# Performance work log

Measured on AMD Instinct MI355X. Metric: run time of the kernel, lower is better.

## Reference

```python
import jax, jax.numpy as jnp
import numpy as np

B, C, Np, D = 16, 64, 128, 128
HT = 4      # time heads
HS = 4      # space heads (GAT)
F = D       # GAT out_channels
DK = D // 2 # q/k proj dim
TOPK = 8
NEG = -1e30

def ln(x, g, b):
    m = x.mean(-1, keepdims=True)
    v = jnp.mean((x - m) ** 2, axis=-1, keepdims=True)
    return (x - m) / jnp.sqrt(v + 1e-5) * g + b

def setup_inputs() -> dict:
    key = jax.random.key(0)
    ks = jax.random.split(key, 16)
    w = lambda k, s: (jax.random.normal(k, s, jnp.float32) * 0.02)
    return dict(
        H_in=jax.random.normal(ks[0], (B, C, Np, D), jnp.float32),
        static_adj=jax.random.normal(ks[1], (C, C), jnp.float32) * 0.1,
        attn_in_w=w(ks[2], (3 * D, D)), attn_in_b=jnp.zeros((3 * D,), jnp.float32),
        attn_out_w=w(ks[3], (D, D)), attn_out_b=jnp.zeros((D,), jnp.float32),
        ln1_g=jnp.ones((D,), jnp.float32), ln1_b=jnp.zeros((D,), jnp.float32),
        ln2_g=jnp.ones((D,), jnp.float32), ln2_b=jnp.zeros((D,), jnp.float32),
        ff1_w=w(ks[4], (4 * D, D)), ff1_b=jnp.zeros((4 * D,), jnp.float32),
        ff2_w=w(ks[5], (D, 4 * D)), ff2_b=jnp.zeros((D,), jnp.float32),
        tnorm_g=jnp.ones((D,), jnp.float32), tnorm_b=jnp.zeros((D,), jnp.float32),
        q_w=w(ks[6], (DK, D)), q_b=jnp.zeros((DK,), jnp.float32),
        k_w=w(ks[7], (DK, D)), k_b=jnp.zeros((DK,), jnp.float32),
        gat_w=w(ks[8], (HS, F, D)),
        gat_att_src=w(ks[9], (HS, F)), gat_att_dst=w(ks[10], (HS, F)),
        gat_bias=jnp.zeros((D,), jnp.float32),
        snorm_g=jnp.ones((D,), jnp.float32), snorm_b=jnp.zeros((D,), jnp.float32),
    )

def _forward(H_in, static_adj, attn_in_w, attn_in_b, attn_out_w, attn_out_b,
             ln1_g, ln1_b, ln2_g, ln2_b, ff1_w, ff1_b, ff2_w, ff2_b,
             tnorm_g, tnorm_b, q_w, q_b, k_w, k_b,
             gat_w, gat_att_src, gat_att_dst, gat_bias, snorm_g, snorm_b):
    dh = D // HT
    # ---- temporal transformer encoder layer (norm_first) on [B*C, Np, D]
    x0 = H_in.reshape(B * C, Np, D)
    h = ln(x0, ln1_g, ln1_b)
    qkv = h @ attn_in_w.T + attn_in_b
    q, k, v = jnp.split(qkv, 3, axis=-1)
    q = q.reshape(-1, Np, HT, dh).transpose(0, 2, 1, 3)
    k = k.reshape(-1, Np, HT, dh).transpose(0, 2, 1, 3)
    v = v.reshape(-1, Np, HT, dh).transpose(0, 2, 1, 3)
    att = jax.nn.softmax(jnp.einsum('nhqd,nhkd->nhqk', q, k) / jnp.sqrt(jnp.float32(dh)), axis=-1)
    o = jnp.einsum('nhqk,nhkd->nhqd', att, v).transpose(0, 2, 1, 3).reshape(-1, Np, D)
    x = x0 + (o @ attn_out_w.T + attn_out_b)
    h2 = ln(x, ln2_g, ln2_b)
    x = x + jax.nn.relu(h2 @ ff1_w.T + ff1_b) @ ff2_w.T + ff2_b
    H_temp = ln(x0 + x, tnorm_g, tnorm_b).reshape(B, C, Np, D)
    # ---- dynamic adjacency from temporal summary
    Hs = H_temp.mean(axis=2)                              # [B,C,D]
    q2 = Hs @ q_w.T + q_b
    k2 = Hs @ k_w.T + k_b
    sim = jnp.einsum('bcd,bed->bce', q2, k2) * (DK ** -0.5)
    A = jnp.tanh(sim) + static_adj[None]                  # [B,C,C]
    # ---- top-k edge mask per sample (row r -> its top-k cols, no self loops)
    kk = max(1, min(TOPK, C - 1))
    idx = jax.lax.top_k(A, kk)[1]                         # [B,C,kk]
    mask = jnp.any(jax.nn.one_hot(idx, C, dtype=bool), axis=2)  # [B,C,C]
    mask = mask & (~jnp.eye(C, dtype=bool)) & (A != 0)
    # ---- dense masked GAT over all (B, Np) graphs; src=row, dst=col
    xh = jnp.einsum('bcpd,hfd->bphcf', H_temp, gat_w)     # [B,Np,HS,C,F]
    asrc = jnp.einsum('bphcf,hf->bphc', xh, gat_att_src)
    adst = jnp.einsum('bphcf,hf->bphc', xh, gat_att_dst)
    e = asrc[..., :, None] + adst[..., None, :]           # [B,Np,HS,src,dst]
    e = jnp.where(e > 0, e, 0.2 * e)                      # LeakyReLU(0.2)
    mb = mask[:, None, None, :, :]
    e = jnp.where(mb, e, NEG)
    e = e - e.max(axis=3, keepdims=True)                  # softmax over src per dst
    wgt = jnp.exp(e) * mb
    s = wgt.sum(axis=3, keepdims=True)
    a = wgt / jnp.where(s > 0, s, 1.0)
    out = jnp.einsum('bphst,bphsf->bphtf', a, xh).mean(axis=2) + gat_bias  # [B,Np,C,F]
    out = out.transpose(0, 2, 1, 3)                       # [B,C,Np,D]
    return ln(out + H_temp, snorm_g, snorm_b)

def reference(H_in, static_adj, attn_in_w, attn_in_b, attn_out_w, attn_out_b,
              ln1_g, ln1_b, ln2_g, ln2_b, ff1_w, ff1_b, ff2_w, ff2_b,
              tnorm_g, tnorm_b, q_w, q_b, k_w, k_b,
              gat_w, gat_att_src, gat_att_dst, gat_bias, snorm_g, snorm_b):
    return _forward(H_in, static_adj, attn_in_w, attn_in_b, attn_out_w, attn_out_b,
                    ln1_g, ln1_b, ln2_g, ln2_b, ff1_w, ff1_b, ff2_w, ff2_b,
                    tnorm_g, tnorm_b, q_w, q_b, k_w, k_b,
                    gat_w, gat_att_src, gat_att_dst, gat_bias, snorm_g, snorm_b)
```

## Files before the change

kernel.cpp:

```cpp
#include <hip/hip_runtime.h>
#include <cstdint>


typedef __attribute__((ext_vector_type(8)))  short bf16x8;
typedef __attribute__((ext_vector_type(16))) float f32x16;
#define MFMA32(a, b, c) __builtin_amdgcn_mfma_f32_32x32x16_bf16((a), (b), (c), 0, 0, 0)

__device__ __forceinline__ unsigned short f2bf(float f) {
    unsigned int u = __float_as_uint(f);
    u += 0x7fffu + ((u >> 16) & 1u);
    return (unsigned short)(u >> 16);
}
__device__ __forceinline__ float bf2f(unsigned short u) {
    return __uint_as_float(((unsigned int)u) << 16);
}

__device__ __forceinline__ bf16x8 lds_frag(const unsigned short* p) {
    union { bf16x8 v; ushort4 h[2]; } u;
    u.h[0] = *(const ushort4*)p;
    u.h[1] = *(const ushort4*)(p + 4);
    return u.v;
}
__device__ __forceinline__ bf16x8 gfrag(const unsigned short* p) {
    union { bf16x8 v; uint4 u; } t;
    t.u = *(const uint4*)p;
    return t.v;
}

__device__ __forceinline__ int rowmap(int r, int hl) { return (r & 3) + 8 * (r >> 2) + 4 * hl; }

__device__ __forceinline__ unsigned int pk2(float lo, float hi) {
    return (unsigned int)f2bf(lo) | ((unsigned int)f2bf(hi) << 16);
}

template<int B>
__device__ __forceinline__ bf16x8 pack_frag(const f32x16& p) {
    unsigned int a0 = pk2(p[B + 0], p[B + 1]);
    unsigned int a1 = pk2(p[B + 2], p[B + 3]);
    unsigned int b0 = pk2(p[B + 4], p[B + 5]);
    unsigned int b1 = pk2(p[B + 6], p[B + 7]);
    asm("v_permlane32_swap_b32 %0, %1" : "+v"(b0), "+v"(a0));
    asm("v_permlane32_swap_b32 %0, %1" : "+v"(b1), "+v"(a1));
    union { bf16x8 v; unsigned int w[4]; } u;
    u.w[0] = a0; u.w[1] = a1; u.w[2] = b0; u.w[3] = b1;
    return u.v;
}

__global__ void wconv_kernel(const float* __restrict__ wqkv, const float* __restrict__ wout,
                             const float* __restrict__ w1, const float* __restrict__ w2,
                             const float* __restrict__ gw,
                             unsigned short* __restrict__ dst) {
    int i = blockIdx.x * 256 + threadIdx.x;
    float v;
    if (i < 49152)       v = wqkv[i];
    else if (i < 65536)  v = wout[i - 49152];
    else if (i < 131072) v = w1[i - 65536];
    else if (i < 196608) v = w2[i - 131072];
    else                 v = gw[i - 196608];
    dst[i] = f2bf(v);
}

__global__ void wa_kernel(const float* __restrict__ gw, const float* __restrict__ asw,
                          const float* __restrict__ adw,
                          float* __restrict__ waS, float* __restrict__ waD) {
    int t = blockIdx.x * 256 + threadIdx.x;
    int h = t >> 8, d = (t >> 1) & 127, which = t & 1;
    const float* av = which ? adw : asw;
    float s = 0.f;
    for (int f = 0; f < 128; f++) s += av[h * 128 + f] * gw[(h * 128 + f) * 128 + d];
    (which ? waD : waS)[h * 128 + d] = s;
}

__global__ __launch_bounds__(256, 2)
void temporal_kernel(const float* __restrict__ Hin,
                     const unsigned short* __restrict__ wqkv_b, const float* __restrict__ bqkv,
                     const unsigned short* __restrict__ wout_b, const float* __restrict__ bout,
                     const float* __restrict__ g1, const float* __restrict__ b1,
                     const float* __restrict__ g2, const float* __restrict__ b2,
                     const unsigned short* __restrict__ w1_b, const float* __restrict__ bf1,
                     const unsigned short* __restrict__ w2_b, const float* __restrict__ bf2,
                     const float* __restrict__ tg, const float* __restrict__ tb,
                     float* __restrict__ Htemp) {
    __shared__ unsigned short RA[128][132];
    __shared__ double RBd[2208];
    unsigned short (*kb)[36]  = (unsigned short(*)[36])RBd;
    unsigned short (*vT)[132] = (unsigned short(*)[132])((char*)RBd + 9216);
    unsigned short (*rscr)[32][36] = (unsigned short(*)[32][36])RBd;

    const int n = blockIdx.x;
    const int tid = threadIdx.x;
    const int lane = tid & 63;
    const int wv = tid >> 6;
    const int hl = lane >> 5;
    const int l31 = lane & 31;
    const int myrow = wv * 32 + l31;

    {
        int row = tid >> 1, hf = tid & 1;
        const float* src = Hin + ((long)n * 128 + row) * 128 + hf * 64;
        float xv[64];
        float s = 0.f, qs = 0.f;
#pragma unroll
        for (int i = 0; i < 64; i += 4) {
            float4 t = *(const float4*)(src + i);
            xv[i] = t.x; xv[i+1] = t.y; xv[i+2] = t.z; xv[i+3] = t.w;
        }
#pragma unroll
        for (int i = 0; i < 64; i++) { s += xv[i]; qs += xv[i] * xv[i]; }
        s += __shfl_xor(s, 1); qs += __shfl_xor(qs, 1);
        float mu = s * 0.0078125f;
        float rs = rsqrtf(fmaxf(qs * 0.0078125f - mu * mu, 0.f) + 1e-5f);
#pragma unroll
        for (int i = 0; i < 64; i++) {
            int d = hf * 64 + i;
            RA[row][d] = f2bf((xv[i] - mu) * rs * g1[d] + b1[d]);
        }
    }

    unsigned int opk[4][8];

#pragma unroll
    for (int h = 0; h < 4; h++) {
        bf16x8 qf0, qf1;
        {
            f32x16 accq, acck, accv;
#pragma unroll
            for (int r = 0; r < 16; r++) accq[r] = bqkv[h * 32 + rowmap(r, hl)];
            float bk = bqkv[128 + h * 32 + l31];
            float bv = bqkv[256 + h * 32 + l31];
#pragma unroll
            for (int r = 0; r < 16; r++) { acck[r] = bk; accv[r] = bv; }
            const unsigned short* wq = wqkv_b + (      h * 32 + l31) * 128 + hl * 8;
            const unsigned short* wk = wqkv_b + (128 + h * 32 + l31) * 128 + hl * 8;
            const unsigned short* wvp= wqkv_b + (256 + h * 32 + l31) * 128 + hl * 8;
#pragma unroll
            for (int k0 = 0; k0 < 128; k0 += 16) {
                bf16x8 a  = lds_frag(&RA[myrow][k0 + hl * 8]);
                accq = MFMA32(gfrag(wq + k0), a, accq);
                acck = MFMA32(a, gfrag(wk + k0), acck);
                accv = MFMA32(a, gfrag(wvp + k0), accv);
            }
#pragma unroll
            for (int r = 0; r < 16; r++) {
                int tok = wv * 32 + rowmap(r, hl);
                kb[tok][l31] = f2bf(acck[r]);
                vT[l31][tok] = f2bf(accv[r]);
            }
            qf0 = pack_frag<0>(accq);
            qf1 = pack_frag<8>(accq);
        }
        __syncthreads();

        f32x16 sacc[4];
#pragma unroll
        for (int t = 0; t < 4; t++)
#pragma unroll
            for (int r = 0; r < 16; r++) sacc[t][r] = 0.f;
#pragma unroll
        for (int t = 0; t < 4; t++) {
            bf16x8 ka0 = lds_frag(&kb[t * 32 + l31][hl * 8]);
            sacc[t] = MFMA32(ka0, qf0, sacc[t]);
            bf16x8 ka1 = lds_frag(&kb[t * 32 + l31][16 + hl * 8]);
            sacc[t] = MFMA32(ka1, qf1, sacc[t]);
        }
        const float scale = 0.17677669529663687f;
        float m0 = -1e30f;
#pragma unroll
        for (int t = 0; t < 4; t++)
#pragma unroll
            for (int r = 0; r < 16; r++) m0 = fmaxf(m0, sacc[t][r]);
        m0 = fmaxf(m0, __shfl_xor(m0, 32));
        float ssum = 0.f;
#pragma unroll
        for (int t = 0; t < 4; t++)
#pragma unroll
            for (int r = 0; r < 16; r++) {
                float e = __expf(scale * (sacc[t][r] - m0));
                sacc[t][r] = e; ssum += e;
            }
        ssum += __shfl_xor(ssum, 32);
        float rinv = 1.f / ssum;
#pragma unroll
        for (int t = 0; t < 4; t++)
#pragma unroll
            for (int r = 0; r < 16; r++) sacc[t][r] *= rinv;

        f32x16 oacc;
#pragma unroll
        for (int r = 0; r < 16; r++) oacc[r] = 0.f;
#pragma unroll
        for (int t = 0; t < 4; t++) {
            bf16x8 pf0 = pack_frag<0>(sacc[t]);
            bf16x8 v0  = lds_frag(&vT[l31][t * 32 + hl * 8]);
            oacc = MFMA32(pf0, v0, oacc);
            bf16x8 pf1 = pack_frag<8>(sacc[t]);
            bf16x8 v1  = lds_frag(&vT[l31][t * 32 + 16 + hl * 8]);
            oacc = MFMA32(pf1, v1, oacc);
        }
#pragma unroll
        for (int j = 0; j < 8; j++) opk[h][j] = pk2(oacc[2*j], oacc[2*j+1]);
        __syncthreads();
    }

#pragma unroll
    for (int h = 0; h < 4; h++)
#pragma unroll
        for (int j = 0; j < 8; j++) {
            int tok0 = wv * 32 + rowmap(2*j,     hl);
            int tok1 = wv * 32 + rowmap(2*j + 1, hl);
            RA[tok0][h * 32 + l31] = (unsigned short)(opk[h][j] & 0xffffu);
            RA[tok1][h * 32 + l31] = (unsigned short)(opk[h][j] >> 16);
        }

    f32x16 acc[4];
#pragma unroll
    for (int t = 0; t < 4; t++) {
        float bo = bout[t * 32 + l31];
#pragma unroll
        for (int r = 0; r < 16; r++) {
            int tok = wv * 32 + rowmap(r, hl);
            acc[t][r] = Hin[((long)n * 128 + tok) * 128 + t * 32 + l31] + bo;
        }
    }
#pragma unroll
    for (int k0 = 0; k0 < 128; k0 += 16) {
        bf16x8 a = lds_frag(&RA[myrow][k0 + hl * 8]);
#pragma unroll
        for (int t = 0; t < 4; t++) {
            bf16x8 b = gfrag(wout_b + (t * 32 + l31) * 128 + k0 + hl * 8);
            acc[t] = MFMA32(a, b, acc[t]);
        }
    }

#pragma unroll
    for (int r = 0; r < 16; r++) {
        float s = acc[0][r] + acc[1][r] + acc[2][r] + acc[3][r];
#pragma unroll
        for (int d = 1; d < 32; d <<= 1) s += __shfl_xor(s, d);
        float mu = s * 0.0078125f;
        float q = 0.f;
#pragma unroll
        for (int t = 0; t < 4; t++) { float dv = acc[t][r] - mu; q += dv * dv; }
#pragma unroll
        for (int d = 1; d < 32; d <<= 1) q += __shfl_xor(q, d);
        float rs = rsqrtf(q * 0.0078125f + 1e-5f);
        int row = wv * 32 + rowmap(r, hl);
#pragma unroll
        for (int t = 0; t < 4; t++) {
            int col = t * 32 + l31;
            RA[row][col] = f2bf((acc[t][r] - mu) * rs * g2[col] + b2[col]);
        }
    }

#pragma unroll
    for (int t = 0; t < 4; t++) {
        float bv = bf2[t * 32 + l31];
#pragma unroll
        for (int r = 0; r < 16; r++) acc[t][r] += bv;
    }

    for (int j = 0; j < 4; j++) {
        f32x16 racc[4];
#pragma unroll
        for (int t = 0; t < 4; t++) {
            float bv = bf1[j * 128 + t * 32 + l31];
#pragma unroll
            for (int r = 0; r < 16; r++) racc[t][r] = bv;
        }
#pragma unroll
        for (int k0 = 0; k0 < 128; k0 += 16) {
            bf16x8 a = lds_frag(&RA[myrow][k0 + hl * 8]);
#pragma unroll
            for (int t = 0; t < 4; t++) {
                bf16x8 b = gfrag(w1_b + (j * 128 + t * 32 + l31) * 128 + k0 + hl * 8);
                racc[t] = MFMA32(a, b, racc[t]);
            }
        }
#pragma unroll
        for (int t = 0; t < 4; t++) {
#pragma unroll
            for (int r = 0; r < 16; r++)
                rscr[wv][rowmap(r, hl)][l31] = f2bf(fmaxf(racc[t][r], 0.f));
#pragma unroll
            for (int kk = 0; kk < 32; kk += 16) {
                bf16x8 a = lds_frag(&rscr[wv][l31][kk + hl * 8]);
#pragma unroll
                for (int tp = 0; tp < 4; tp++) {
                    bf16x8 b = gfrag(w2_b + (tp * 32 + l31) * 512 + j * 128 + t * 32 + kk + hl * 8);
                    acc[tp] = MFMA32(a, b, acc[tp]);
                }
            }
        }
    }

#pragma unroll
    for (int t = 0; t < 4; t++)
#pragma unroll
        for (int r = 0; r < 16; r++) {
            int tok = wv * 32 + rowmap(r, hl);
            acc[t][r] += Hin[((long)n * 128 + tok) * 128 + t * 32 + l31];
        }
    float* outf = Htemp + (long)n * 16384;
#pragma unroll
    for (int r = 0; r < 16; r++) {
        float s = acc[0][r] + acc[1][r] + acc[2][r] + acc[3][r];
#pragma unroll
        for (int d = 1; d < 32; d <<= 1) s += __shfl_xor(s, d);
        float mu = s * 0.0078125f;
        float q = 0.f;
#pragma unroll
        for (int t = 0; t < 4; t++) { float dv = acc[t][r] - mu; q += dv * dv; }
#pragma unroll
        for (int d = 1; d < 32; d <<= 1) q += __shfl_xor(q, d);
        float rs = rsqrtf(q * 0.0078125f + 1e-5f);
        int tok = wv * 32 + rowmap(r, hl);
#pragma unroll
        for (int t = 0; t < 4; t++) {
            int col = t * 32 + l31;
            outf[tok * 128 + col] = (acc[t][r] - mu) * rs * tg[col] + tb[col];
        }
    }
}

__global__ void hs_kernel(const float* __restrict__ Htemp, float* __restrict__ Hs) {
    int idx = blockIdx.x * 256 + threadIdx.x;
    int n = idx >> 7, d = idx & 127;
    float s = 0.f;
    for (int p = 0; p < 128; p++) s += Htemp[((long)n * 128 + p) * 128 + d];
    Hs[idx] = s * 0.0078125f;
}

__global__ __launch_bounds__(256)
void graph_kernel(const float* __restrict__ Hs,
                  const float* __restrict__ qw, const float* __restrict__ qb,
                  const float* __restrict__ kw, const float* __restrict__ kb,
                  const float* __restrict__ adj, unsigned long long* __restrict__ masks) {
    __shared__ float q2l[64][65];
    __shared__ float k2l[64][65];
    __shared__ float am[64][65];
    int b = blockIdx.x;
    int tid = threadIdx.x;
    {
        int r = tid & 127, jh = tid >> 7;
        int row = r & 63;
        const float* wmat = (r < 64) ? qw : kw;
        const float* bvec = (r < 64) ? qb : kb;
        const float* src = Hs + (long)(b * 64 + row) * 128;
        for (int jj = 0; jj < 32; jj++) {
            int j = jh * 32 + jj;
            const float* wrow = wmat + (long)j * 128;
            float s0 = 0.f, s1 = 0.f, s2 = 0.f, s3 = 0.f;
#pragma unroll
            for (int d = 0; d < 128; d += 4) {
                s0 += src[d] * wrow[d];     s1 += src[d+1] * wrow[d+1];
                s2 += src[d+2] * wrow[d+2]; s3 += src[d+3] * wrow[d+3];
            }
            float val = ((s0 + s1) + (s2 + s3)) + bvec[j];
            if (r < 64) q2l[row][j] = val; else k2l[row][j] = val;
        }
    }
    __syncthreads();
    {
        int c = tid & 63, eq = tid >> 6;
        for (int ee = 0; ee < 16; ee++) {
            int e = eq * 16 + ee;
            float s0 = 0.f, s1 = 0.f, s2 = 0.f, s3 = 0.f;
#pragma unroll
            for (int j = 0; j < 64; j += 4) {
                s0 += q2l[c][j]   * k2l[e][j];
                s1 += q2l[c][j+1] * k2l[e][j+1];
                s2 += q2l[c][j+2] * k2l[e][j+2];
                s3 += q2l[c][j+3] * k2l[e][j+3];
            }
            float sim = ((s0 + s1) + (s2 + s3)) * 0.125f;
            am[c][e] = tanhf(sim) + adj[c * 64 + e];
        }
    }
    __syncthreads();
    if (tid < 64) {
        int c = tid;
        unsigned long long sel = 0ull;
        for (int it = 0; it < 8; it++) {
            float best = -1e38f; int bi = 0;
            for (int e = 0; e < 64; e++) {
                float v = am[c][e];
                bool ok = (((sel >> e) & 1ull) == 0ull) && (v > best);
                best = ok ? v : best;
                bi = ok ? e : bi;
            }
            sel |= (1ull << bi);
        }
        sel &= ~(1ull << c);
        for (int e = 0; e < 64; e++)
            if (am[c][e] == 0.f) sel &= ~(1ull << e);
        masks[b * 64 + c] = sel;
    }
}

__global__ __launch_bounds__(256, 1)
void gat_kernel(float* __restrict__ Htemp,
                const unsigned short* __restrict__ gwb,
                const float* __restrict__ waS, const float* __restrict__ waD,
                const float* __restrict__ gbias,
                const unsigned long long* __restrict__ masks,
                const float* __restrict__ sg, const float* __restrict__ sb) {
    __shared__ unsigned short Htb[64][132];
    __shared__ double ovl_d[3264];
    __shared__ float asrcF[4][64], adstF[4][64];
    __shared__ float pmax[4][64], psum[4][64];
    __shared__ unsigned long long mk[64];

    unsigned short (*xhT)[68]  = (unsigned short(*)[68])ovl_d;
    unsigned short (*attT)[68] = (unsigned short(*)[68])((char*)ovl_d + 17408);
    float (*part)[8][64]       = (float(*)[8][64])ovl_d;

    const int bp = blockIdx.x;
    const int b = bp >> 7, p = bp & 127;
    const int tid = threadIdx.x;
    const int lane = tid & 63, wv = tid >> 6;
    const int hl = lane >> 5, l31 = lane & 31;
    const int rs = (wv & 1) * 32;
    const int cs = (wv >> 1) * 64;

    {
        int c = tid >> 2, qq = tid & 3;
        const float* src = Htemp + ((long)(b * 64 + c) * 128 + p) * 128 + qq * 32;
#pragma unroll
        for (int k = 0; k < 8; k++) {
            float4 t4 = *(const float4*)(src + 4 * k);
            ushort4 u; u.x = f2bf(t4.x); u.y = f2bf(t4.y); u.z = f2bf(t4.z); u.w = f2bf(t4.w);
            *(ushort4*)&Htb[c][qq * 32 + 4 * k] = u;
        }
    }
    if (tid < 64) mk[tid] = masks[b * 64 + tid];
    __syncthreads();

    {
        int s = lane, q = wv;
        float acc[8];
#pragma unroll
        for (int m = 0; m < 8; m++) acc[m] = 0.f;
        const unsigned int* hp = (const unsigned int*)&Htb[s][q * 32];
#pragma unroll
        for (int d2 = 0; d2 < 16; d2++) {
            unsigned int u = hp[d2];
            float f0 = __uint_as_float(u << 16);
            float f1 = __uint_as_float(u & 0xffff0000u);
            int d = q * 32 + 2 * d2;
#pragma unroll
            for (int h = 0; h < 4; h++) {
                acc[2*h]   += f0 * waS[h * 128 + d] + f1 * waS[h * 128 + d + 1];
                acc[2*h+1] += f0 * waD[h * 128 + d] + f1 * waD[h * 128 + d + 1];
            }
        }
#pragma unroll
        for (int m = 0; m < 8; m++) part[q][m][s] = acc[m];
    }
    __syncthreads();
    for (int o = tid; o < 512; o += 256) {
        int h = o >> 7, rem = o & 127, which = rem >> 6, s = rem & 63;
        int m = h * 2 + which;
        float v = part[0][m][s] + part[1][m][s] + part[2][m][s] + part[3][m][s];
        if (which == 0) asrcF[h][s] = v; else adstF[h][s] = v;
    }
    __syncthreads();

    f32x16 oacc0, oacc1;
#pragma unroll
    for (int r = 0; r < 16; r++) { oacc0[r] = 0.f; oacc1[r] = 0.f; }

    for (int h = 0; h < 4; h++) {
        f32x16 a0, a1;
#pragma unroll
        for (int r = 0; r < 16; r++) { a0[r] = 0.f; a1[r] = 0.f; }
        const unsigned short* gwh = gwb + h * 16384;
#pragma unroll
        for (int k0 = 0; k0 < 128; k0 += 16) {
            bf16x8 af = lds_frag(&Htb[rs + l31][k0 + hl * 8]);
            bf16x8 b0 = gfrag(gwh + (cs + l31) * 128 + k0 + hl * 8);
            bf16x8 b1 = gfrag(gwh + (cs + 32 + l31) * 128 + k0 + hl * 8);
            a0 = MFMA32(af, b0, a0);
            a1 = MFMA32(af, b1, a1);
        }
#pragma unroll
        for (int g = 0; g < 4; g++) {
            ushort4 u0, u1;
            u0.x = f2bf(a0[4*g]);   u0.y = f2bf(a0[4*g+1]);
            u0.z = f2bf(a0[4*g+2]); u0.w = f2bf(a0[4*g+3]);
            u1.x = f2bf(a1[4*g]);   u1.y = f2bf(a1[4*g+1]);
            u1.z = f2bf(a1[4*g+2]); u1.w = f2bf(a1[4*g+3]);
            int so = rs + 4 * hl + 8 * g;
            *(ushort4*)&xhT[cs + l31][so]      = u0;
            *(ushort4*)&xhT[cs + 32 + l31][so] = u1;
        }
        __syncthreads();

        {
            int t = lane;
            float adv = adstF[h][t];
            float ev[16];
            float mx = -1e30f;
#pragma unroll
            for (int i = 0; i < 16; i++) {
                int s = wv * 16 + i;
                float e = asrcF[h][s] + adv;
                e = (e > 0.f) ? e : 0.2f * e;
                ev[i] = e;
                if ((mk[s] >> t) & 1ull) mx = fmaxf(mx, e);
            }
            pmax[wv][t] = mx;
            __syncthreads();
            float M = fmaxf(fmaxf(pmax[0][t], pmax[1][t]), fmaxf(pmax[2][t], pmax[3][t]));
            float sm = 0.f;
#pragma unroll
            for (int i = 0; i < 16; i++) {
                int s = wv * 16 + i;
                float w = ((mk[s] >> t) & 1ull) ? __expf(ev[i] - M) : 0.f;
                ev[i] = w; sm += w;
            }
            psum[wv][t] = sm;
            __syncthreads();
            float S = psum[0][t] + psum[1][t] + psum[2][t] + psum[3][t];
            float rinv = (S > 0.f) ? 1.f / S : 0.f;
#pragma unroll
            for (int g = 0; g < 4; g++) {
                ushort4 u;
                u.x = f2bf(ev[4*g]   * rinv); u.y = f2bf(ev[4*g+1] * rinv);
                u.z = f2bf(ev[4*g+2] * rinv); u.w = f2bf(ev[4*g+3] * rinv);
                *(ushort4*)&attT[t][wv * 16 + 4 * g] = u;
            }
        }
        __syncthreads();

#pragma unroll
        for (int k0 = 0; k0 < 64; k0 += 16) {
            bf16x8 af = lds_frag(&attT[rs + l31][k0 + hl * 8]);
            bf16x8 b0 = lds_frag(&xhT[cs + l31][k0 + hl * 8]);
            bf16x8 b1 = lds_frag(&xhT[cs + 32 + l31][k0 + hl * 8]);
            oacc0 = MFMA32(af, b0, oacc0);
            oacc1 = MFMA32(af, b1, oacc1);
        }
        __syncthreads();
    }

    float gb0 = gbias[cs + l31], gb1 = gbias[cs + 32 + l31];
    float v0[16], v1[16];
#pragma unroll
    for (int r = 0; r < 16; r++) {
        int c = rs + rowmap(r, hl);
        v0[r] = oacc0[r] * 0.25f + gb0 + bf2f(Htb[c][cs + l31]);
        v1[r] = oacc1[r] * 0.25f + gb1 + bf2f(Htb[c][cs + 32 + l31]);
    }
#pragma unroll
    for (int r = 0; r < 16; r++) {
        float s = v0[r] + v1[r];
        float q = v0[r] * v0[r] + v1[r] * v1[r];
#pragma unroll
        for (int d = 1; d < 32; d <<= 1) { s += __shfl_xor(s, d); q += __shfl_xor(q, d); }
        if (l31 == 0) {
            int c = rs + rowmap(r, hl);
            pmax[wv >> 1][c] = s;
            psum[wv >> 1][c] = q;
        }
    }
    __syncthreads();
    float sgv0 = sg[cs + l31], sbv0 = sb[cs + l31];
    float sgv1 = sg[cs + 32 + l31], sbv1 = sb[cs + 32 + l31];
#pragma unroll
    for (int r = 0; r < 16; r++) {
        int c = rs + rowmap(r, hl);
        float sum = pmax[0][c] + pmax[1][c];
        float sq  = psum[0][c] + psum[1][c];
        float mu = sum * 0.0078125f;
        float var = sq * 0.0078125f - mu * mu;
        float rsd = rsqrtf(fmaxf(var, 0.f) + 1e-5f);
        float* orow = Htemp + ((long)(b * 64 + c) * 128 + p) * 128;
        orow[cs + l31]      = (v0[r] - mu) * rsd * sgv0 + sbv0;
        orow[cs + 32 + l31] = (v1[r] - mu) * rsd * sgv1 + sbv1;
    }
}

extern "C" void kernel_launch(void* const* d_in, const int* in_sizes, int n_in,
                              void* d_out, int out_size, void* d_ws, size_t ws_size,
                              hipStream_t stream) {
    const float* Hin        = (const float*)d_in[0];
    const float* static_adj = (const float*)d_in[1];
    const float* attn_in_w  = (const float*)d_in[2];
    const float* attn_in_b  = (const float*)d_in[3];
    const float* attn_out_w = (const float*)d_in[4];
    const float* attn_out_b = (const float*)d_in[5];
    const float* ln1_g      = (const float*)d_in[6];
    const float* ln1_b      = (const float*)d_in[7];
    const float* ln2_g      = (const float*)d_in[8];
    const float* ln2_b      = (const float*)d_in[9];
    const float* ff1_w      = (const float*)d_in[10];
    const float* ff1_b      = (const float*)d_in[11];
    const float* ff2_w      = (const float*)d_in[12];
    const float* ff2_b      = (const float*)d_in[13];
    const float* tnorm_g    = (const float*)d_in[14];
    const float* tnorm_b    = (const float*)d_in[15];
    const float* q_w        = (const float*)d_in[16];
    const float* q_b        = (const float*)d_in[17];
    const float* k_w        = (const float*)d_in[18];
    const float* k_b        = (const float*)d_in[19];
    const float* gat_w      = (const float*)d_in[20];
    const float* gat_att_src= (const float*)d_in[21];
    const float* gat_att_dst= (const float*)d_in[22];
    const float* gat_bias   = (const float*)d_in[23];
    const float* snorm_g    = (const float*)d_in[24];
    const float* snorm_b    = (const float*)d_in[25];

    float* out = (float*)d_out;
    char* ws = (char*)d_ws;
    unsigned short* wb = (unsigned short*)ws;
    const unsigned short* wqkv_b = wb;
    const unsigned short* wout_b = wb + 49152;
    const unsigned short* w1_b   = wb + 65536;
    const unsigned short* w2_b   = wb + 131072;
    const unsigned short* gw_b   = wb + 196608;
    unsigned long long* masks = (unsigned long long*)(ws + 524288);
    float* Hs  = (float*)(ws + 532480);
    float* waS = (float*)(ws + 1056768);
    float* waD = (float*)(ws + 1058816);

    hipLaunchKernelGGL(wconv_kernel, dim3(1024), dim3(256), 0, stream,
                       attn_in_w, attn_out_w, ff1_w, ff2_w, gat_w, wb);
    hipLaunchKernelGGL(wa_kernel, dim3(4), dim3(256), 0, stream,
                       gat_w, gat_att_src, gat_att_dst, waS, waD);
    hipLaunchKernelGGL(temporal_kernel, dim3(1024), dim3(256), 0, stream,
                       Hin, wqkv_b, attn_in_b, wout_b, attn_out_b,
                       ln1_g, ln1_b, ln2_g, ln2_b,
                       w1_b, ff1_b, w2_b, ff2_b, tnorm_g, tnorm_b, out);
    hipLaunchKernelGGL(hs_kernel, dim3(512), dim3(256), 0, stream, out, Hs);
    hipLaunchKernelGGL(graph_kernel, dim3(16), dim3(256), 0, stream,
                       Hs, q_w, q_b, k_w, k_b, static_adj, masks);
    hipLaunchKernelGGL(gat_kernel, dim3(2048), dim3(256), 0, stream,
                       out, gw_b, waS, waD, gat_bias,
                       masks, snorm_g, snorm_b);
}
```

Before: 576.9 us.

## Double-buffer per-head QKV with attention and fuse time-mean into temporal kernel

The per-head loop in the temporal kernel now uses two K/V LDS buffers, so the QKV projection for the next head is issued while the current head's softmax and PV run, and one barrier per head is dropped. The token mean (Hs) is computed inside the temporal epilogue through a small LDS reduction, which removes the separate hs_kernel pass that re-read all of Htemp. The GAT kernel's launch bounds are raised to two blocks per CU. In exchange, LDS use and register pressure in the temporal kernel go up, which could lower occupancy or cause spills.

```diff
diff --git a/kernel.cpp b/kernel.cpp
--- a/kernel.cpp
+++ b/kernel.cpp
@@ -71,6 +71,71 @@
     (which ? waD : waS)[h * 128 + d] = s;
 }
 
+#define QKV_STAGE(H, KBB, VTB) do {                                              \
+    f32x16 accq, acck, accv;                                                     \
+    _Pragma("unroll") for (int r = 0; r < 16; r++)                               \
+        accq[r] = bqkv[(H) * 32 + rowmap(r, hl)];                                \
+    float bk_ = bqkv[128 + (H) * 32 + l31];                                      \
+    float bv_ = bqkv[256 + (H) * 32 + l31];                                      \
+    _Pragma("unroll") for (int r = 0; r < 16; r++) { acck[r] = bk_; accv[r] = bv_; } \
+    const unsigned short* wq_ = wqkv_b + ((H) * 32 + l31) * 128 + hl * 8;        \
+    const unsigned short* wk_ = wqkv_b + (128 + (H) * 32 + l31) * 128 + hl * 8;  \
+    const unsigned short* wv_ = wqkv_b + (256 + (H) * 32 + l31) * 128 + hl * 8;  \
+    _Pragma("unroll") for (int k0 = 0; k0 < 128; k0 += 16) {                     \
+        bf16x8 a_ = lds_frag(&RA[myrow][k0 + hl * 8]);                           \
+        accq = MFMA32(gfrag(wq_ + k0), a_, accq);   \
+        acck = MFMA32(a_, gfrag(wk_ + k0), acck);                                \
+        accv = MFMA32(a_, gfrag(wv_ + k0), accv);                                \
+    }                                                                            \
+    _Pragma("unroll") for (int r = 0; r < 16; r++) {                             \
+        int tok_ = wv * 32 + rowmap(r, hl);                                      \
+        KBB[tok_][l31] = f2bf(acck[r]);                                          \
+        VTB[l31][tok_] = f2bf(accv[r]);                                          \
+    }                                                                            \
+    qf0_ = pack_frag<0>(accq);                                                   \
+    qf1_ = pack_frag<8>(accq);                                                   \
+} while (0)
+
+#define ATTN_PHASE(H, KBB, VTB, NEXTQKV) do {                                    \
+    f32x16 sacc[4];                                                              \
+    _Pragma("unroll") for (int t = 0; t < 4; t++)                                \
+    _Pragma("unroll") for (int r = 0; r < 16; r++) sacc[t][r] = 0.f;             \
+    _Pragma("unroll") for (int t = 0; t < 4; t++) {                              \
+        bf16x8 ka0 = lds_frag(&KBB[t * 32 + l31][hl * 8]);                       \
+        sacc[t] = MFMA32(ka0, qf0_, sacc[t]);                                    \
+        bf16x8 ka1 = lds_frag(&KBB[t * 32 + l31][16 + hl * 8]);                  \
+        sacc[t] = MFMA32(ka1, qf1_, sacc[t]);                                    \
+    }                                                                            \
+    NEXTQKV;                                                                     \
+    const float scale_ = 0.17677669529663687f;                   \
+    float m0 = -1e30f;                                                           \
+    _Pragma("unroll") for (int t = 0; t < 4; t++)                                \
+    _Pragma("unroll") for (int r = 0; r < 16; r++) m0 = fmaxf(m0, sacc[t][r]);   \
+    m0 = fmaxf(m0, __shfl_xor(m0, 32));                                          \
+    float ssum = 0.f;                                                            \
+    _Pragma("unroll") for (int t = 0; t < 4; t++)                                \
+    _Pragma("unroll") for (int r = 0; r < 16; r++) {                             \
+        float e_ = __expf(scale_ * (sacc[t][r] - m0));                           \
+        sacc[t][r] = e_; ssum += e_;                                             \
+    }                                                                            \
+    ssum += __shfl_xor(ssum, 32);                                                \
+    float rinv_ = 1.f / ssum;                                                    \
+    _Pragma("unroll") for (int t = 0; t < 4; t++)                                \
+    _Pragma("unroll") for (int r = 0; r < 16; r++) sacc[t][r] *= rinv_;          \
+    f32x16 oacc;                                                                 \
+    _Pragma("unroll") for (int r = 0; r < 16; r++) oacc[r] = 0.f;                \
+    _Pragma("unroll") for (int t = 0; t < 4; t++) {                              \
+        bf16x8 pf0 = pack_frag<0>(sacc[t]);                                      \
+        bf16x8 v0_ = lds_frag(&VTB[l31][t * 32 + hl * 8]);                       \
+        oacc = MFMA32(pf0, v0_, oacc);                                           \
+        bf16x8 pf1 = pack_frag<8>(sacc[t]);                                      \
+        bf16x8 v1_ = lds_frag(&VTB[l31][t * 32 + 16 + hl * 8]);                  \
+        oacc = MFMA32(pf1, v1_, oacc);                                           \
+    }                                                                            \
+    _Pragma("unroll") for (int j = 0; j < 8; j++)                                \
+        opk[H][j] = pk2(oacc[2*j], oacc[2*j+1]);                                 \
+} while (0)
+
 __global__ __launch_bounds__(256, 2)
 void temporal_kernel(const float* __restrict__ Hin,
                      const unsigned short* __restrict__ wqkv_b, const float* __restrict__ bqkv,
@@ -80,12 +145,15 @@
                      const unsigned short* __restrict__ w1_b, const float* __restrict__ bf1,
                      const unsigned short* __restrict__ w2_b, const float* __restrict__ bf2,
                      const float* __restrict__ tg, const float* __restrict__ tb,
-                     float* __restrict__ Htemp) {
+                     float* __restrict__ Htemp, float* __restrict__ Hs) {
     __shared__ unsigned short RA[128][132];
-    __shared__ double RBd[2208];
-    unsigned short (*kb)[36]  = (unsigned short(*)[36])RBd;
-    unsigned short (*vT)[132] = (unsigned short(*)[132])((char*)RBd + 9216);
+    __shared__ double RBd[4416];
+    unsigned short (*kb0)[36]  = (unsigned short(*)[36])RBd;
+    unsigned short (*vT0)[132] = (unsigned short(*)[132])((char*)RBd + 9216);
+    unsigned short (*kb1)[36]  = (unsigned short(*)[36])((char*)RBd + 17664);
+    unsigned short (*vT1)[132] = (unsigned short(*)[132])((char*)RBd + 26880);
     unsigned short (*rscr)[32][36] = (unsigned short(*)[32][36])RBd;
+    float (*hsred)[128] = (float(*)[128])((char*)RBd + 9216);
 
     const int n = blockIdx.x;
     const int tid = threadIdx.x;
@@ -118,89 +186,17 @@
     }
 
     unsigned int opk[4][8];
-
-#pragma unroll
-    for (int h = 0; h < 4; h++) {
-        bf16x8 qf0, qf1;
-        {
-            f32x16 accq, acck, accv;
-#pragma unroll
-            for (int r = 0; r < 16; r++) accq[r] = bqkv[h * 32 + rowmap(r, hl)];
-            float bk = bqkv[128 + h * 32 + l31];
-            float bv = bqkv[256 + h * 32 + l31];
-#pragma unroll
-            for (int r = 0; r < 16; r++) { acck[r] = bk; accv[r] = bv; }
-            const unsigned short* wq = wqkv_b + (      h * 32 + l31) * 128 + hl * 8;
-            const unsigned short* wk = wqkv_b + (128 + h * 32 + l31) * 128 + hl * 8;
-            const unsigned short* wvp= wqkv_b + (256 + h * 32 + l31) * 128 + hl * 8;
-#pragma unroll
-            for (int k0 = 0; k0 < 128; k0 += 16) {
-                bf16x8 a  = lds_frag(&RA[myrow][k0 + hl * 8]);
-                accq = MFMA32(gfrag(wq + k0), a, accq);
-                acck = MFMA32(a, gfrag(wk + k0), acck);
-                accv = MFMA32(a, gfrag(wvp + k0), accv);
-            }
-#pragma unroll
-            for (int r = 0; r < 16; r++) {
-                int tok = wv * 32 + rowmap(r, hl);
-                kb[tok][l31] = f2bf(acck[r]);
-                vT[l31][tok] = f2bf(accv[r]);
-            }
-            qf0 = pack_frag<0>(accq);
-            qf1 = pack_frag<8>(accq);
-        }
-        __syncthreads();
-
-        f32x16 sacc[4];
-#pragma unroll
-        for (int t = 0; t < 4; t++)
-#pragma unroll
-            for (int r = 0; r < 16; r++) sacc[t][r] = 0.f;
-#pragma unroll
-        for (int t = 0; t < 4; t++) {
-            bf16x8 ka0 = lds_frag(&kb[t * 32 + l31][hl * 8]);
-            sacc[t] = MFMA32(ka0, qf0, sacc[t]);
-            bf16x8 ka1 = lds_frag(&kb[t * 32 + l31][16 + hl * 8]);
-            sacc[t] = MFMA32(ka1, qf1, sacc[t]);
-        }
-        const float scale = 0.17677669529663687f;
-        float m0 = -1e30f;
-#pragma unroll
-        for (int t = 0; t < 4; t++)
-#pragma unroll
-            for (int r = 0; r < 16; r++) m0 = fmaxf(m0, sacc[t][r]);
-        m0 = fmaxf(m0, __shfl_xor(m0, 32));
-        float ssum = 0.f;
-#pragma unroll
-        for (int t = 0; t < 4; t++)
-#pragma unroll
-            for (int r = 0; r < 16; r++) {
-                float e = __expf(scale * (sacc[t][r] - m0));
-                sacc[t][r] = e; ssum += e;
-            }
-        ssum += __shfl_xor(ssum, 32);
-        float rinv = 1.f / ssum;
-#pragma unroll
-        for (int t = 0; t < 4; t++)
-#pragma unroll
-            for (int r = 0; r < 16; r++) sacc[t][r] *= rinv;
-
-        f32x16 oacc;
-#pragma unroll
-        for (int r = 0; r < 16; r++) oacc[r] = 0.f;
-#pragma unroll
-        for (int t = 0; t < 4; t++) {
-            bf16x8 pf0 = pack_frag<0>(sacc[t]);
-            bf16x8 v0  = lds_frag(&vT[l31][t * 32 + hl * 8]);
-            oacc = MFMA32(pf0, v0, oacc);
-            bf16x8 pf1 = pack_frag<8>(sacc[t]);
-            bf16x8 v1  = lds_frag(&vT[l31][t * 32 + 16 + hl * 8]);
-            oacc = MFMA32(pf1, v1, oacc);
-        }
-#pragma unroll
-        for (int j = 0; j < 8; j++) opk[h][j] = pk2(oacc[2*j], oacc[2*j+1]);
-        __syncthreads();
-    }
+    bf16x8 qf0_, qf1_;
+
+    QKV_STAGE(0, kb0, vT0);
+    __syncthreads();
+    ATTN_PHASE(0, kb0, vT0, QKV_STAGE(1, kb1, vT1));
+    __syncthreads();
+    ATTN_PHASE(1, kb1, vT1, QKV_STAGE(2, kb0, vT0));
+    __syncthreads();
+    ATTN_PHASE(2, kb0, vT0, QKV_STAGE(3, kb1, vT1));
+    __syncthreads();
+    ATTN_PHASE(3, kb1, vT1, (void)0);
 
 #pragma unroll
     for (int h = 0; h < 4; h++)
@@ -301,6 +297,7 @@
             acc[t][r] += Hin[((long)n * 128 + tok) * 128 + t * 32 + l31];
         }
     float* outf = Htemp + (long)n * 16384;
+    float cs0 = 0.f, cs1 = 0.f, cs2 = 0.f, cs3 = 0.f;
 #pragma unroll
     for (int r = 0; r < 16; r++) {
         float s = acc[0][r] + acc[1][r] + acc[2][r] + acc[3][r];
@@ -314,20 +311,35 @@
         for (int d = 1; d < 32; d <<= 1) q += __shfl_xor(q, d);
         float rs = rsqrtf(q * 0.0078125f + 1e-5f);
         int tok = wv * 32 + rowmap(r, hl);
-#pragma unroll
-        for (int t = 0; t < 4; t++) {
-            int col = t * 32 + l31;
-            outf[tok * 128 + col] = (acc[t][r] - mu) * rs * tg[col] + tb[col];
-        }
-    }
-}
-
-__global__ void hs_kernel(const float* __restrict__ Htemp, float* __restrict__ Hs) {
-    int idx = blockIdx.x * 256 + threadIdx.x;
-    int n = idx >> 7, d = idx & 127;
-    float s = 0.f;
-    for (int p = 0; p < 128; p++) s += Htemp[((long)n * 128 + p) * 128 + d];
-    Hs[idx] = s * 0.0078125f;
+        {
+            float v = (acc[0][r] - mu) * rs * tg[0 * 32 + l31] + tb[0 * 32 + l31];
+            outf[tok * 128 + 0 * 32 + l31] = v;  cs0 += v;
+        }
+        {
+            float v = (acc[1][r] - mu) * rs * tg[1 * 32 + l31] + tb[1 * 32 + l31];
+            outf[tok * 128 + 1 * 32 + l31] = v;  cs1 += v;
+        }
+        {
+            float v = (acc[2][r] - mu) * rs * tg[2 * 32 + l31] + tb[2 * 32 + l31];
+            outf[tok * 128 + 2 * 32 + l31] = v;  cs2 += v;
+        }
+        {
+            float v = (acc[3][r] - mu) * rs * tg[3 * 32 + l31] + tb[3 * 32 + l31];
+            outf[tok * 128 + 3 * 32 + l31] = v;  cs3 += v;
+        }
+    }
+    cs0 += __shfl_xor(cs0, 32); cs1 += __shfl_xor(cs1, 32);
+    cs2 += __shfl_xor(cs2, 32); cs3 += __shfl_xor(cs3, 32);
+    if (hl == 0) {
+        hsred[wv][0 * 32 + l31] = cs0;
+        hsred[wv][1 * 32 + l31] = cs1;
+        hsred[wv][2 * 32 + l31] = cs2;
+        hsred[wv][3 * 32 + l31] = cs3;
+    }
+    __syncthreads();
+    if (tid < 128)
+        Hs[(long)n * 128 + tid] =
+            (hsred[0][tid] + hsred[1][tid] + hsred[2][tid] + hsred[3][tid]) * 0.0078125f;
 }
 
 __global__ __launch_bounds__(256)
@@ -397,7 +409,7 @@
     }
 }
 
-__global__ __launch_bounds__(256, 1)
+__global__ __launch_bounds__(256, 2)
 void gat_kernel(float* __restrict__ Htemp,
                 const unsigned short* __restrict__ gwb,
                 const float* __restrict__ waS, const float* __restrict__ waD,
@@ -630,8 +642,7 @@
     hipLaunchKernelGGL(temporal_kernel, dim3(1024), dim3(256), 0, stream,
                        Hin, wqkv_b, attn_in_b, wout_b, attn_out_b,
                        ln1_g, ln1_b, ln2_g, ln2_b,
-                       w1_b, ff1_b, w2_b, ff2_b, tnorm_g, tnorm_b, out);
-    hipLaunchKernelGGL(hs_kernel, dim3(512), dim3(256), 0, stream, out, Hs);
+                       w1_b, ff1_b, w2_b, ff2_b, tnorm_g, tnorm_b, out, Hs);
     hipLaunchKernelGGL(graph_kernel, dim3(16), dim3(256), 0, stream,
                        Hs, q_w, q_b, k_w, k_b, static_adj, masks);
     hipLaunchKernelGGL(gat_kernel, dim3(2048), dim3(256), 0, stream,
```

Result: faster. 552.9 us (-4.2%).
